# Optimization experiments

Hardware: AMD Instinct MI355X
Metric: run time of the kernel (lower is better)

The kernel has to match this reference:

```python
import jax, jax.numpy as jnp
import numpy as np

T, N, E = 10, 10000, 320000
IN_C, HID_C, OUT_C = 128, 128, 64
K = 3


def _edge_weights(src, dst, n):
    # PyG ChebConv norm with sym normalization, lambda_max=2:
    # L_hat = -D^{-1/2} A D^{-1/2} (self loops removed, diagonal 0)
    valid = (src != dst).astype(jnp.float32)  # remove_self_loops
    deg = jax.ops.segment_sum(valid, src, num_segments=n)
    dinv = jnp.where(deg > 0, jax.lax.rsqrt(jnp.maximum(deg, 1.0)), 0.0)
    return -valid * dinv[src] * dinv[dst]  # [E]


def _agg(w, src, dst, x, n):
    # (L_hat @ x): messages from src to dst
    return jax.ops.segment_sum(w[:, None] * x[src], dst, num_segments=n)


def _cheb(x, W, b, w, src, dst, n):
    # ChebConv K=3: T0=x, T1=L_hat x, T2=2 L_hat T1 - T0
    Tx0 = x
    Tx1 = _agg(w, src, dst, Tx0, n)
    Tx2 = 2.0 * _agg(w, src, dst, Tx1, n) - Tx0
    return Tx0 @ W[0] + Tx1 @ W[1] + Tx2 @ W[2] + b


def setup_inputs() -> dict:
    key = jax.random.key(0)
    ks = jax.random.split(key, 20)
    features_seq = jax.random.normal(ks[0], (T, N, IN_C), dtype=jnp.float32)
    edges_seq = jax.random.randint(ks[1], (T, 2, E), 0, N, dtype=jnp.int64)
    s = 0.05
    inp = {"features_seq": features_seq, "edges_seq": edges_seq}
    names = ["Wxz", "Whz", "Wxr", "Whr", "Wxh", "Whh"]
    ins = [IN_C, HID_C, IN_C, HID_C, IN_C, HID_C]
    for i, (nm, ci) in enumerate(zip(names, ins)):
        inp[nm] = jax.random.normal(ks[2 + i], (K, ci, HID_C), dtype=jnp.float32) * s
        inp["b" + nm[1:].lower()] = jnp.zeros((HID_C,), dtype=jnp.float32)
    inp["Wp"] = jax.random.normal(ks[10], (HID_C, OUT_C), dtype=jnp.float32) * s
    inp["bp"] = jnp.zeros((OUT_C,), dtype=jnp.float32)
    return inp


def reference(features_seq, edges_seq, Wxz, bxz, Whz, bhz, Wxr, bxr, Whr, bhr,
              Wxh, bxh, Whh, bhh, Wp, bp):
    n = features_seq.shape[1]

    def step(h, xt_et):
        x, e = xt_et
        src, dst = e[0], e[1]
        w = _edge_weights(src, dst, n)
        z = jax.nn.sigmoid(_cheb(x, Wxz, bxz, w, src, dst, n)
                           + _cheb(h, Whz, bhz, w, src, dst, n))
        r = jax.nn.sigmoid(_cheb(x, Wxr, bxr, w, src, dst, n)
                           + _cheb(h, Whr, bhr, w, src, dst, n))
        h_tilde = jnp.tanh(_cheb(x, Wxh, bxh, w, src, dst, n)
                           + _cheb(h * r, Whh, bhh, w, src, dst, n))
        h_new = z * h + (1.0 - z) * h_tilde
        return h_new, None

    h0 = jnp.zeros((n, HID_C), dtype=features_seq.dtype)
    h, _ = jax.lax.scan(step, h0, (features_seq, edges_seq))
    return h @ Wp + bp
```

## Files before the change

kernel.cpp:

```cpp
#include <hip/hip_runtime.h>

#define T_STEPS 10
#define NN 10000
#define EE 320000
#define CC 128
#define NC (NN*CC)
#define BHIST 32
#define EPB (EE/BHIST)
#define NCHK 40
#define PRS 8
#define PES 4
#define PROWS (NN/PRS)
#define PEDG (EE/PES)

typedef unsigned short u16;
typedef unsigned int u32;
typedef __attribute__((ext_vector_type(8))) short bf16x8;
typedef __attribute__((ext_vector_type(4))) float f32x4;

__device__ __forceinline__ float sigmoidf_(float x){ return 1.f/(1.f+__expf(-x)); }
__device__ __forceinline__ float tanhf_(float x){
  x = fminf(15.f, fmaxf(-15.f, x));
  float e = __expf(2.f*x);
  return (e-1.f)/(e+1.f);
}
__device__ __forceinline__ u16 f2bf(float f){
  u32 u = __float_as_uint(f);
  u32 r = u + 0x7fffu + ((u>>16)&1u);
  return (u16)(r>>16);
}
__device__ __forceinline__ float bf2f(u16 s){
  return __uint_as_float(((u32)s)<<16);
}
__device__ __forceinline__ float blo(u32 u){ return __uint_as_float(u<<16); }
__device__ __forceinline__ float bhi(u32 u){ return __uint_as_float(u & 0xffff0000u); }
__device__ __forceinline__ void gload16(const void* g, void* l){
  __builtin_amdgcn_global_load_lds(
    (const __attribute__((address_space(1))) void*)g,
    (__attribute__((address_space(3))) void*)l, 16, 0, 0);
}

__global__ __launch_bounds__(256) void prep_kernel(
    const float* __restrict__ Wxz, const float* __restrict__ Whz,
    const float* __restrict__ Wxr, const float* __restrict__ Whr,
    const float* __restrict__ Wxh, const float* __restrict__ Whh,
    const float* __restrict__ bxz, const float* __restrict__ bhz,
    const float* __restrict__ bxr, const float* __restrict__ bhr,
    const float* __restrict__ bxh, const float* __restrict__ bhh,
    const float* __restrict__ Wp,
    u16* __restrict__ WbigT, u16* __restrict__ WrT, u16* __restrict__ WpT,
    float* __restrict__ bz, float* __restrict__ br, float* __restrict__ bht,
    u16* __restrict__ h)
{
  int idx = blockIdx.x*256 + threadIdx.x;
  if (idx < NC) h[idx] = 0;
  if (idx < 384*768) {
    int c = idx / 768, k = idx - c*768;
    int gate = c >> 7, cc = c & 127;
    int hside = (k >= 384);
    int kk = hside ? k - 384 : k;
    int blk = kk >> 7, row = kk & 127;
    const float* W = nullptr;
    if (!hside) W = (gate==0) ? Wxz : (gate==1) ? Wxr : Wxh;
    else if (gate==0) W = Whz; else if (gate==1) W = Whr;
    float v = 0.f;
    if (W) {
      int base = row*CC + cc;
      float w0 = W[base], w1 = W[CC*CC + base], w2 = W[2*CC*CC + base];
      v = (blk==0) ? (w0 - w2) : (blk==1) ? w1 : (2.f*w2);
    }
    WbigT[idx] = f2bf(v);
  }
  if (idx < 128*384) {
    int c = idx / 384, k = idx - c*384;
    int blk = k >> 7, row = k & 127;
    int base = row*CC + c;
    float w0 = Whh[base], w1 = Whh[CC*CC+base], w2 = Whh[2*CC*CC+base];
    WrT[idx] = f2bf((blk==0) ? (w0-w2) : (blk==1) ? w1 : (2.f*w2));
  }
  if (idx < 64*128) {
    int c = idx >> 7, k = idx & 127;
    WpT[idx] = f2bf(Wp[k*64 + c]);
  }
  if (idx < CC) {
    bz[idx]  = bxz[idx] + bhz[idx];
    br[idx]  = bxr[idx] + bhr[idx];
    bht[idx] = bxh[idx] + bhh[idx];
  }
}

__global__ __launch_bounds__(256) void xconv_kernel(const float* __restrict__ x, u16* __restrict__ xb, int n4){
  int i = blockIdx.x*256 + threadIdx.x;
  if (i >= n4) return;
  long long o = (long long)i*4;
  float4 v = *(const float4*)(x + o);
  u32 u0 = (u32)f2bf(v.x) | ((u32)f2bf(v.y)<<16);
  u32 u1 = (u32)f2bf(v.z) | ((u32)f2bf(v.w)<<16);
  uint2 r; r.x=u0; r.y=u1;
  *(uint2*)(xb + o) = r;
}

__global__ __launch_bounds__(512) void hist_kernel(const int* __restrict__ edges,
                                                   u32* __restrict__ histP){
  __shared__ u32 hist[NN];
  int t = blockIdx.y, b = blockIdx.x, tid = threadIdx.x;
  for (int i = tid; i < NN; i += 512) hist[i] = 0;
  __syncthreads();
  const int* src = edges + (size_t)t*2*EE;
  const int* dst = src + EE;
  int e1 = b*EPB + EPB;
  #pragma unroll 4
  for (int e = b*EPB + tid; e < e1; e += 512){
    int s = src[e], d = dst[e];
    if (s != d){
      atomicAdd(&hist[s], 1u);
      atomicAdd(&hist[d], 1u << 16);
    }
  }
  __syncthreads();
  u32* hp = histP + ((size_t)t*BHIST + b)*NN;
  for (int i = tid; i < NN; i += 512) hp[i] = hist[i];
}

__global__ __launch_bounds__(256) void reduce_scan_kernel(u32* __restrict__ histP,
                                                          int* __restrict__ rowptr_all,
                                                          int* __restrict__ chunk_tot,
                                                          float* __restrict__ dinv_all){
  int t = blockIdx.y, ch = blockIdx.x, tid = threadIdx.x;
  int d = ch*256 + tid;
  u32 run=0, degs=0;
  if (d < NN){
    size_t base = (size_t)t*BHIST*NN + d;
    #pragma unroll
    for (int b=0;b<BHIST;++b){
      size_t ix = base + (size_t)b*NN;
      u32 v = histP[ix];
      histP[ix] = (v & 0xffffu) | (run<<16);
      run += v>>16;
      degs += v & 0xffffu;
    }
    dinv_all[t*NN+d] = degs>0 ? rsqrtf((float)degs) : 0.f;
  }
  int lane = tid&63, wv = tid>>6;
  int s = (int)run;
  #pragma unroll
  for (int off=1; off<64; off<<=1){
    int u = __shfl_up(s, off, 64);
    if (lane>=off) s += u;
  }
  __shared__ int wsum[4];
  if (lane==63) wsum[wv] = s;
  __syncthreads();
  int add = 0;
  #pragma unroll
  for (int w=0; w<3; ++w) if (w < wv) add += wsum[w];
  int incl = s + add;
  if (d < NN) rowptr_all[(size_t)t*(NN+1)+d] = incl - (int)run;
  if (tid==255) chunk_tot[t*NCHK + ch] = incl;
}

__global__ __launch_bounds__(64) void scanb_kernel(const int* __restrict__ chunk_tot,
                                                   int* __restrict__ chunk_base,
                                                   int* __restrict__ rowptr_all){
  int t = blockIdx.x; int lane = threadIdx.x;
  int v = (lane < NCHK) ? chunk_tot[t*NCHK+lane] : 0;
  int s = v;
  #pragma unroll
  for (int off=1; off<64; off<<=1){
    int u = __shfl_up(s, off, 64);
    if (lane>=off) s += u;
  }
  if (lane < NCHK) chunk_base[t*NCHK+lane] = s - v;
  if (lane == NCHK-1) rowptr_all[(size_t)t*(NN+1)+NN] = s;
}

__global__ __launch_bounds__(256) void scanc_kernel(int* __restrict__ rowptr_all,
                                                    const int* __restrict__ chunk_base){
  int t = blockIdx.y, ch = blockIdx.x;
  int d = ch*256 + threadIdx.x;
  if (d < NN) rowptr_all[(size_t)t*(NN+1)+d] += chunk_base[t*NCHK+ch];
}

__global__ __launch_bounds__(512) void place_kernel(const int* __restrict__ edges,
                                                    const int* __restrict__ rowptr_all,
                                                    const u32* __restrict__ histP,
                                                    u16* __restrict__ colA_all){
  __shared__ int slot[PROWS];
  int t = blockIdx.y, b = blockIdx.x, tid = threadIdx.x;
  int rs = b >> 2, es = b & 3;
  int lo = rs*PROWS, hi = lo + PROWS;
  const int* rowptr = rowptr_all + (size_t)t*(NN+1);
  const u32* hp = histP + ((size_t)t*BHIST + es*8)*NN;
  for (int i = tid; i < PROWS; i += 512)
    slot[i] = rowptr[lo+i] + (int)(hp[lo+i] >> 16);
  __syncthreads();
  const int* src = edges + (size_t)t*2*EE;
  const int* dst = src + EE;
  u16* colA = colA_all + (size_t)t*EE;
  int e1 = es*PEDG + PEDG;
  #pragma unroll 4
  for (int e = es*PEDG + tid; e < e1; e += 512){
    int d = dst[e];
    if (d >= lo && d < hi){
      int s = src[e];
      if (s != d){
        int pos = atomicAdd(&slot[d-lo], 1);
        colA[pos] = (u16)s;
      }
    }
  }
}

__device__ __forceinline__ void spmm_row4(const int* __restrict__ rowptr, const u16* __restrict__ colA,
                                          const float* __restrict__ dinv,
                                          const u16* __restrict__ in, u16* __restrict__ out,
                                          int wb, int wave, int lane){
  int row = wb*4 + wave;
  int k0 = rowptr[row], k1 = rowptr[row+1];
  int q = lane >> 4, cl = lane & 15;
  float a0=0.f,a1=0.f,a2=0.f,a3=0.f,a4=0.f,a5=0.f,a6=0.f,a7=0.f;
  #pragma unroll 2
  for (int k = k0 + q; k < k1; k += 4){
    int s = colA[k];
    float w = dinv[s];
    uint4 u = *(const uint4*)(in + (size_t)s*CC + cl*8);
    a0 = fmaf(w, blo(u.x), a0);  a1 = fmaf(w, bhi(u.x), a1);
    a2 = fmaf(w, blo(u.y), a2);  a3 = fmaf(w, bhi(u.y), a3);
    a4 = fmaf(w, blo(u.z), a4);  a5 = fmaf(w, bhi(u.z), a5);
    a6 = fmaf(w, blo(u.w), a6);  a7 = fmaf(w, bhi(u.w), a7);
  }
  a0 += __shfl_xor(a0,16); a1 += __shfl_xor(a1,16);
  a2 += __shfl_xor(a2,16); a3 += __shfl_xor(a3,16);
  a4 += __shfl_xor(a4,16); a5 += __shfl_xor(a5,16);
  a6 += __shfl_xor(a6,16); a7 += __shfl_xor(a7,16);
  a0 += __shfl_xor(a0,32); a1 += __shfl_xor(a1,32);
  a2 += __shfl_xor(a2,32); a3 += __shfl_xor(a3,32);
  a4 += __shfl_xor(a4,32); a5 += __shfl_xor(a5,32);
  a6 += __shfl_xor(a6,32); a7 += __shfl_xor(a7,32);
  if (q == 0){
    float wrow = -dinv[row];
    uint4 r;
    r.x = (u32)f2bf(wrow*a0) | ((u32)f2bf(wrow*a1)<<16);
    r.y = (u32)f2bf(wrow*a2) | ((u32)f2bf(wrow*a3)<<16);
    r.z = (u32)f2bf(wrow*a4) | ((u32)f2bf(wrow*a5)<<16);
    r.w = (u32)f2bf(wrow*a6) | ((u32)f2bf(wrow*a7)<<16);
    *(uint4*)(out + (size_t)row*CC + cl*8) = r;
  }
}

__global__ __launch_bounds__(256) void spmm_kernel(const int* __restrict__ rowptr, const u16* __restrict__ colA,
                                                   const float* __restrict__ dinv,
                                                   const u16* __restrict__ in, u16* __restrict__ out){
  int wave = threadIdx.x >> 6, lane = threadIdx.x & 63;
  int wb = blockIdx.x;
  if (wb >= NN/4) return;
  spmm_row4(rowptr, colA, dinv, in, out, wb, wave, lane);
}

__global__ __launch_bounds__(256) void spmm2_kernel(const int* __restrict__ rowptr, const u16* __restrict__ colA,
                                                    const float* __restrict__ dinv,
                                                    const u16* __restrict__ in0, u16* __restrict__ out0,
                                                    const u16* __restrict__ in1, u16* __restrict__ out1){
  int wave = threadIdx.x >> 6, lane = threadIdx.x & 63;
  int bid = blockIdx.x;
  int xcd = bid & 7;
  int inp = xcd >> 2;
  int wb  = (bid >> 3)*4 + (xcd & 3);
  if (wb >= NN/4) return;
  spmm_row4(rowptr, colA, dinv, inp?in1:in0, inp?out1:out0, wb, wave, lane);
}

template<int NSEG, int KDIM, int EPI, int SWZN>
__global__ __launch_bounds__(256) void mgemm_kernel(
    const u16* __restrict__ A0, const u16* __restrict__ A1, const u16* __restrict__ A2,
    const u16* __restrict__ A3, const u16* __restrict__ A4, const u16* __restrict__ A5,
    const u16* __restrict__ Bt,
    const float* __restrict__ bias0, const float* __restrict__ bias1,
    const u16* __restrict__ hbuf,
    float* __restrict__ zbuf, float* __restrict__ chx,
    u16* __restrict__ hr_out, u16* __restrict__ h_out,
    float* __restrict__ out_f)
{
  __shared__ __align__(16) u16 As[64*128];
  __shared__ __align__(16) u16 Bs[64*128];
  const u16* segs[6] = {A0,A1,A2,A3,A4,A5};
  int tid = threadIdx.x, lane = tid & 63, wvi = tid >> 6;
  int m0, n0;
  if (SWZN > 0){
    int bid = blockIdx.x;
    int j = bid >> 3;
    int mt = (bid & 7)*20 + (j % 20);
    if (mt >= 157) return;
    m0 = mt*64; n0 = (j/20)*64;
  } else {
    m0 = blockIdx.x*64; n0 = blockIdx.y*64;
  }
  int wr = wvi >> 1, wc = wvi & 1;

  f32x4 acc[2][2] = {};

  int c_lo = wvi*64 + lane;
  int rl = lane & 15, rg = lane >> 4;
  int offA[2][4], offB[2][4];
  #pragma unroll
  for (int mf=0; mf<2; ++mf)
    #pragma unroll
    for (int ks=0; ks<4; ++ks){
      offA[mf][ks] = (wr*32 + mf*16 + rl)*256 + ((((ks<<2)+rg) ^ rl)<<4);
      offB[mf][ks] = (wc*32 + mf*16 + rl)*256 + ((((ks<<2)+rg) ^ rl)<<4);
    }

  const int ktend = (EPI==1 && n0 >= 256) ? (NSEG/2) : NSEG;
  for (int kt=0; kt<ktend; ++kt){
    const u16* __restrict__ Aseg = segs[kt];
    __syncthreads();
    #pragma unroll
    for (int i=0;i<4;++i){
      int c = i*256 + c_lo;
      int row = c >> 4, slot = c & 15;
      int scw = slot ^ (row & 15);
      int grow = m0 + row; if (grow > NN-1) grow = NN-1;
      gload16(Aseg + (size_t)grow*CC + scw*8,
              (u16*)As + ((size_t)i*256 + wvi*64)*8);
      gload16(Bt + (size_t)(n0 + row)*KDIM + kt*128 + scw*8,
              (u16*)Bs + ((size_t)i*256 + wvi*64)*8);
    }
    __syncthreads();
    #pragma unroll
    for (int ks=0; ks<4; ++ks){
      bf16x8 a0 = *(const bf16x8*)((const char*)As + offA[0][ks]);
      bf16x8 a1 = *(const bf16x8*)((const char*)As + offA[1][ks]);
      bf16x8 b0 = *(const bf16x8*)((const char*)Bs + offB[0][ks]);
      bf16x8 b1 = *(const bf16x8*)((const char*)Bs + offB[1][ks]);
      acc[0][0] = __builtin_amdgcn_mfma_f32_16x16x32_bf16(a0, b0, acc[0][0], 0,0,0);
      acc[0][1] = __builtin_amdgcn_mfma_f32_16x16x32_bf16(a0, b1, acc[0][1], 0,0,0);
      acc[1][0] = __builtin_amdgcn_mfma_f32_16x16x32_bf16(a1, b0, acc[1][0], 0,0,0);
      acc[1][1] = __builtin_amdgcn_mfma_f32_16x16x32_bf16(a1, b1, acc[1][1], 0,0,0);
    }
  }

  #pragma unroll
  for (int mf=0; mf<2; ++mf){
    #pragma unroll
    for (int nf=0; nf<2; ++nf){
      #pragma unroll
      for (int r=0; r<4; ++r){
        int grow = m0 + wr*32 + mf*16 + rg*4 + r;
        if (grow >= NN) continue;
        int gcol = n0 + wc*32 + nf*16 + rl;
        float v = acc[mf][nf][r];
        if (EPI==0){
          out_f[(size_t)grow*64 + gcol] = v + bias0[gcol];
        } else if (EPI==1){
          int gate = gcol >> 7, c = gcol & 127;
          size_t idx = (size_t)grow*CC + c;
          if (gate==0)      zbuf[idx] = sigmoidf_(v + bias0[c]);
          else if (gate==1){
            float rr = sigmoidf_(v + bias1[c]);
            hr_out[idx] = f2bf(rr * bf2f(hbuf[idx]));
          } else            chx[idx] = v;
        } else {
          size_t idx = (size_t)grow*CC + gcol;
          float pre = v + chx[idx] + bias0[gcol];
          float ht = tanhf_(pre);
          float zz = zbuf[idx];
          float hv = bf2f(hbuf[idx]);
          h_out[idx] = f2bf(fmaf(zz, hv - ht, ht));
        }
      }
    }
  }
}

extern "C" void kernel_launch(void* const* d_in, const int* in_sizes, int n_in,
                              void* d_out, int out_size, void* d_ws, size_t ws_size,
                              hipStream_t stream)
{
  (void)in_sizes; (void)n_in; (void)out_size; (void)ws_size;
  const float* feat = (const float*)d_in[0];
  const int*   edges = (const int*)d_in[1];
  const float* Wxz=(const float*)d_in[2];  const float* bxz=(const float*)d_in[3];
  const float* Whz=(const float*)d_in[4];  const float* bhz=(const float*)d_in[5];
  const float* Wxr=(const float*)d_in[6];  const float* bxr=(const float*)d_in[7];
  const float* Whr=(const float*)d_in[8];  const float* bhr=(const float*)d_in[9];
  const float* Wxh=(const float*)d_in[10]; const float* bxh=(const float*)d_in[11];
  const float* Whh=(const float*)d_in[12]; const float* bhh=(const float*)d_in[13];
  const float* Wp =(const float*)d_in[14]; const float* bp =(const float*)d_in[15];
  float* out = (float*)d_out;

  char* p = (char*)d_ws;
  auto alloc = [&](size_t bytes)->char* {
    char* r = p; p += (bytes + 255) & ~(size_t)255; return r;
  };
  u16* xb   = (u16*)alloc((size_t)T_STEPS*NC*2);
  u16* h    = (u16*)alloc((size_t)NC*2);
  u16* a1x  = (u16*)alloc((size_t)NC*2);
  u16* a2x  = (u16*)alloc((size_t)NC*2);
  u16* a1h  = (u16*)alloc((size_t)NC*2);
  u16* a2h  = (u16*)alloc((size_t)NC*2);
  u16* hr   = (u16*)alloc((size_t)NC*2);
  float* zbuf = (float*)alloc((size_t)NC*4);
  float* chx  = (float*)alloc((size_t)NC*4);
  u16* WbigT = (u16*)alloc(384*768*2);
  u16* WrT   = (u16*)alloc(128*384*2);
  u16* WpT   = (u16*)alloc(64*128*2);
  float* bz  = (float*)alloc(CC*4);
  float* br  = (float*)alloc(CC*4);
  float* bht = (float*)alloc(CC*4);
  float* dinv_all = (float*)alloc((size_t)T_STEPS*NN*4);
  int* rowptr_all = (int*)alloc((size_t)T_STEPS*(NN+1)*4);
  u16* colA_all   = (u16*)alloc((size_t)T_STEPS*EE*2);
  int* chunk_tot  = (int*)alloc((size_t)T_STEPS*NCHK*4);
  int* chunk_base = (int*)alloc((size_t)T_STEPS*NCHK*4);
  u32* histP = (u32*)hr;

  prep_kernel<<<NC/256, 256, 0, stream>>>(Wxz,Whz,Wxr,Whr,Wxh,Whh,
                                          bxz,bhz,bxr,bhr,bxh,bhh, Wp,
                                          WbigT, WrT, WpT, bz, br, bht, h);
  xconv_kernel<<<(T_STEPS*NC/4 + 255)/256, 256, 0, stream>>>(feat, xb, T_STEPS*NC/4);

  hist_kernel<<<dim3(BHIST, T_STEPS), 512, 0, stream>>>(edges, histP);
  reduce_scan_kernel<<<dim3(NCHK, T_STEPS), 256, 0, stream>>>(histP, rowptr_all, chunk_tot, dinv_all);
  scanb_kernel<<<T_STEPS, 64, 0, stream>>>(chunk_tot, chunk_base, rowptr_all);
  scanc_kernel<<<dim3(NCHK, T_STEPS), 256, 0, stream>>>(rowptr_all, chunk_base);
  place_kernel<<<dim3(PRS*PES, T_STEPS), 512, 0, stream>>>(edges, rowptr_all, histP, colA_all);

  for (int t=0; t<T_STEPS; ++t){
    const int*   rowptr = rowptr_all + (size_t)t*(NN+1);
    const u16*   colA   = colA_all + (size_t)t*EE;
    const float* dinv   = dinv_all + (size_t)t*NN;
    const u16*   x      = xb + (size_t)t*NC;

    spmm2_kernel<<<dim3(2*(NN/4)), 256, 0, stream>>>(rowptr,colA,dinv, x,a1x, h,a1h);
    spmm2_kernel<<<dim3(2*(NN/4)), 256, 0, stream>>>(rowptr,colA,dinv, a1x,a2x, a1h,a2h);

    mgemm_kernel<6,768,1,6><<<dim3(8*20*6), 256, 0, stream>>>(
        x,a1x,a2x,h,a1h,a2h, WbigT, bz, br, h, zbuf, chx, hr, nullptr, nullptr);

    spmm_kernel<<<dim3(NN/4), 256, 0, stream>>>(rowptr,colA,dinv, hr, a1x);
    spmm_kernel<<<dim3(NN/4), 256, 0, stream>>>(rowptr,colA,dinv, a1x, a2x);

    mgemm_kernel<3,384,2,2><<<dim3(8*20*2), 256, 0, stream>>>(
        hr,a1x,a2x,nullptr,nullptr,nullptr, WrT, bht, nullptr, h, zbuf, chx,
        nullptr, h, nullptr);
  }

  mgemm_kernel<1,128,0,0><<<dim3(157,1), 256, 0, stream>>>(
      h,nullptr,nullptr,nullptr,nullptr,nullptr, WpT, bp, nullptr,
      nullptr, nullptr, nullptr, nullptr, nullptr, out);
}
```

Before: 923.7 us.

## Batch input-feature Chebyshev aggregations for all timesteps before the recurrent loop

The x-side sparse aggregations (L_hat x and L_hat^2 x) do not depend on the hidden state, so they are hoisted out of the time loop and computed for all ten timesteps in two large batched launches, with per-timestep result buffers. Inside the loop only the hidden-state aggregations remain, run with the single-input spmm kernel. Separately, the edge placement kernel now gives each block a full-row shared slot table and its own edge chunk, replacing the row-range/edge-split scheme. This trades extra workspace memory for fewer serial small launches and better GPU fill, and changes the parallel decomposition of placement.

Result: faster. 898.8 us (-2.7%).

```diff
diff --git a/kernel.cpp b/kernel.cpp
--- a/kernel.cpp
+++ b/kernel.cpp
@@ -8,10 +8,6 @@
 #define BHIST 32
 #define EPB (EE/BHIST)
 #define NCHK 40
-#define PRS 8
-#define PES 4
-#define PROWS (NN/PRS)
-#define PEDG (EE/PES)
 
 typedef unsigned short u16;
 typedef unsigned int u32;
@@ -185,28 +181,22 @@
                                                     const int* __restrict__ rowptr_all,
                                                     const u32* __restrict__ histP,
                                                     u16* __restrict__ colA_all){
-  __shared__ int slot[PROWS];
+  __shared__ int slot[NN];
   int t = blockIdx.y, b = blockIdx.x, tid = threadIdx.x;
-  int rs = b >> 2, es = b & 3;
-  int lo = rs*PROWS, hi = lo + PROWS;
   const int* rowptr = rowptr_all + (size_t)t*(NN+1);
-  const u32* hp = histP + ((size_t)t*BHIST + es*8)*NN;
-  for (int i = tid; i < PROWS; i += 512)
-    slot[i] = rowptr[lo+i] + (int)(hp[lo+i] >> 16);
+  const u32* hp = histP + ((size_t)t*BHIST + b)*NN;
+  for (int i = tid; i < NN; i += 512) slot[i] = rowptr[i] + (int)(hp[i] >> 16);
   __syncthreads();
   const int* src = edges + (size_t)t*2*EE;
   const int* dst = src + EE;
   u16* colA = colA_all + (size_t)t*EE;
-  int e1 = es*PEDG + PEDG;
+  int e1 = b*EPB + EPB;
   #pragma unroll 4
-  for (int e = es*PEDG + tid; e < e1; e += 512){
-    int d = dst[e];
-    if (d >= lo && d < hi){
-      int s = src[e];
-      if (s != d){
-        int pos = atomicAdd(&slot[d-lo], 1);
-        colA[pos] = (u16)s;
-      }
+  for (int e = b*EPB + tid; e < e1; e += 512){
+    int s = src[e], d = dst[e];
+    if (s != d){
+      int pos = atomicAdd(&slot[d], 1);
+      colA[pos] = (u16)s;
     }
   }
 }
@@ -257,17 +247,23 @@
   spmm_row4(rowptr, colA, dinv, in, out, wb, wave, lane);
 }
 
-__global__ __launch_bounds__(256) void spmm2_kernel(const int* __restrict__ rowptr, const u16* __restrict__ colA,
-                                                    const float* __restrict__ dinv,
-                                                    const u16* __restrict__ in0, u16* __restrict__ out0,
-                                                    const u16* __restrict__ in1, u16* __restrict__ out1){
-  int wave = threadIdx.x >> 6, lane = threadIdx.x & 63;
+__global__ __launch_bounds__(256) void bxchain_kernel(const int* __restrict__ rowptr_all,
+                                                      const u16* __restrict__ colA_all,
+                                                      const float* __restrict__ dinv_all,
+                                                      const u16* __restrict__ in_all,
+                                                      u16* __restrict__ out_all){
+  int lane = threadIdx.x & 63, wave = threadIdx.x >> 6;
   int bid = blockIdx.x;
   int xcd = bid & 7;
-  int inp = xcd >> 2;
-  int wb  = (bid >> 3)*4 + (xcd & 3);
-  if (wb >= NN/4) return;
-  spmm_row4(rowptr, colA, dinv, inp?in1:in0, inp?out1:out0, wb, wave, lane);
+  int j = bid >> 3;
+  int t, wb;
+  if (j < 2500){ t = xcd; wb = j; }
+  else { t = 8 + (xcd >> 2); wb = (j - 2500)*4 + (xcd & 3); }
+  const int*   rowptr = rowptr_all + (size_t)t*(NN+1);
+  const u16*   colA   = colA_all + (size_t)t*EE;
+  const float* dinv   = dinv_all + (size_t)t*NN;
+  spmm_row4(rowptr, colA, dinv, in_all + (size_t)t*NC, out_all + (size_t)t*NC,
+            wb, wave, lane);
 }
 
 template<int NSEG, int KDIM, int EPI, int SWZN>
@@ -392,10 +388,10 @@
   auto alloc = [&](size_t bytes)->char* {
     char* r = p; p += (bytes + 255) & ~(size_t)255; return r;
   };
-  u16* xb   = (u16*)alloc((size_t)T_STEPS*NC*2);
+  u16* xb     = (u16*)alloc((size_t)T_STEPS*NC*2);
+  u16* a1xA   = (u16*)alloc((size_t)T_STEPS*NC*2);
+  u16* a2xA   = (u16*)alloc((size_t)T_STEPS*NC*2);
   u16* h    = (u16*)alloc((size_t)NC*2);
-  u16* a1x  = (u16*)alloc((size_t)NC*2);
-  u16* a2x  = (u16*)alloc((size_t)NC*2);
   u16* a1h  = (u16*)alloc((size_t)NC*2);
   u16* a2h  = (u16*)alloc((size_t)NC*2);
   u16* hr   = (u16*)alloc((size_t)NC*2);
@@ -423,16 +419,21 @@
   reduce_scan_kernel<<<dim3(NCHK, T_STEPS), 256, 0, stream>>>(histP, rowptr_all, chunk_tot, dinv_all);
   scanb_kernel<<<T_STEPS, 64, 0, stream>>>(chunk_tot, chunk_base, rowptr_all);
   scanc_kernel<<<dim3(NCHK, T_STEPS), 256, 0, stream>>>(rowptr_all, chunk_base);
-  place_kernel<<<dim3(PRS*PES, T_STEPS), 512, 0, stream>>>(edges, rowptr_all, histP, colA_all);
+  place_kernel<<<dim3(BHIST, T_STEPS), 512, 0, stream>>>(edges, rowptr_all, histP, colA_all);
+
+  bxchain_kernel<<<dim3(25000), 256, 0, stream>>>(rowptr_all, colA_all, dinv_all, xb, a1xA);
+  bxchain_kernel<<<dim3(25000), 256, 0, stream>>>(rowptr_all, colA_all, dinv_all, a1xA, a2xA);
 
   for (int t=0; t<T_STEPS; ++t){
     const int*   rowptr = rowptr_all + (size_t)t*(NN+1);
     const u16*   colA   = colA_all + (size_t)t*EE;
     const float* dinv   = dinv_all + (size_t)t*NN;
     const u16*   x      = xb + (size_t)t*NC;
-
-    spmm2_kernel<<<dim3(2*(NN/4)), 256, 0, stream>>>(rowptr,colA,dinv, x,a1x, h,a1h);
-    spmm2_kernel<<<dim3(2*(NN/4)), 256, 0, stream>>>(rowptr,colA,dinv, a1x,a2x, a1h,a2h);
+    u16* a1x = a1xA + (size_t)t*NC;
+    u16* a2x = a2xA + (size_t)t*NC;
+
+    spmm_kernel<<<dim3(NN/4), 256, 0, stream>>>(rowptr,colA,dinv, h, a1h);
+    spmm_kernel<<<dim3(NN/4), 256, 0, stream>>>(rowptr,colA,dinv, a1h, a2h);
 
     mgemm_kernel<6,768,1,6><<<dim3(8*20*6), 256, 0, stream>>>(
         x,a1x,a2x,h,a1h,a2h, WbigT, bz, br, h, zbuf, chx, hr, nullptr, nullptr);
```

## Simplify edge placement to per-histogram-block slots and widen SpMM lane work to 16 channels

Applied to the files above, without the earlier changes.

The place kernel stops partitioning by row range and edge slice. Each block now handles one histogram block's edge chunk, keeps slot counters for all 10000 rows in shared memory (40KB), and drops the per-edge row-range filter. The SpMM row routine now has each lane cover 16 channels with two 16-byte loads and walk 8 edges in parallel instead of 4, adding one more shuffle-reduction level. The intent is fewer redundant edge reads during placement and more memory parallelism per wave in the gather. The costs are higher register pressure from 16 accumulators and lower occupancy for the place kernel because of its large shared array.

Result: faster. 883.6 us (-4.3%).

```diff
diff --git a/kernel.cpp b/kernel.cpp
--- a/kernel.cpp
+++ b/kernel.cpp
@@ -8,10 +8,6 @@
 #define BHIST 32
 #define EPB (EE/BHIST)
 #define NCHK 40
-#define PRS 8
-#define PES 4
-#define PROWS (NN/PRS)
-#define PEDG (EE/PES)
 
 typedef unsigned short u16;
 typedef unsigned int u32;
@@ -185,28 +181,22 @@
                                                     const int* __restrict__ rowptr_all,
                                                     const u32* __restrict__ histP,
                                                     u16* __restrict__ colA_all){
-  __shared__ int slot[PROWS];
+  __shared__ int slot[NN];
   int t = blockIdx.y, b = blockIdx.x, tid = threadIdx.x;
-  int rs = b >> 2, es = b & 3;
-  int lo = rs*PROWS, hi = lo + PROWS;
   const int* rowptr = rowptr_all + (size_t)t*(NN+1);
-  const u32* hp = histP + ((size_t)t*BHIST + es*8)*NN;
-  for (int i = tid; i < PROWS; i += 512)
-    slot[i] = rowptr[lo+i] + (int)(hp[lo+i] >> 16);
+  const u32* hp = histP + ((size_t)t*BHIST + b)*NN;
+  for (int i = tid; i < NN; i += 512) slot[i] = rowptr[i] + (int)(hp[i] >> 16);
   __syncthreads();
   const int* src = edges + (size_t)t*2*EE;
   const int* dst = src + EE;
   u16* colA = colA_all + (size_t)t*EE;
-  int e1 = es*PEDG + PEDG;
+  int e1 = b*EPB + EPB;
   #pragma unroll 4
-  for (int e = es*PEDG + tid; e < e1; e += 512){
-    int d = dst[e];
-    if (d >= lo && d < hi){
-      int s = src[e];
-      if (s != d){
-        int pos = atomicAdd(&slot[d-lo], 1);
-        colA[pos] = (u16)s;
-      }
+  for (int e = b*EPB + tid; e < e1; e += 512){
+    int s = src[e], d = dst[e];
+    if (s != d){
+      int pos = atomicAdd(&slot[d], 1);
+      colA[pos] = (u16)s;
     }
   }
 }
@@ -217,34 +207,45 @@
                                           int wb, int wave, int lane){
   int row = wb*4 + wave;
   int k0 = rowptr[row], k1 = rowptr[row+1];
-  int q = lane >> 4, cl = lane & 15;
-  float a0=0.f,a1=0.f,a2=0.f,a3=0.f,a4=0.f,a5=0.f,a6=0.f,a7=0.f;
+  int q = lane >> 3, cl = lane & 7;
+  float a[16];
+  #pragma unroll
+  for (int i=0;i<16;++i) a[i]=0.f;
   #pragma unroll 2
-  for (int k = k0 + q; k < k1; k += 4){
+  for (int k = k0 + q; k < k1; k += 8){
     int s = colA[k];
     float w = dinv[s];
-    uint4 u = *(const uint4*)(in + (size_t)s*CC + cl*8);
-    a0 = fmaf(w, blo(u.x), a0);  a1 = fmaf(w, bhi(u.x), a1);
-    a2 = fmaf(w, blo(u.y), a2);  a3 = fmaf(w, bhi(u.y), a3);
-    a4 = fmaf(w, blo(u.z), a4);  a5 = fmaf(w, bhi(u.z), a5);
-    a6 = fmaf(w, blo(u.w), a6);  a7 = fmaf(w, bhi(u.w), a7);
-  }
-  a0 += __shfl_xor(a0,16); a1 += __shfl_xor(a1,16);
-  a2 += __shfl_xor(a2,16); a3 += __shfl_xor(a3,16);
-  a4 += __shfl_xor(a4,16); a5 += __shfl_xor(a5,16);
-  a6 += __shfl_xor(a6,16); a7 += __shfl_xor(a7,16);
-  a0 += __shfl_xor(a0,32); a1 += __shfl_xor(a1,32);
-  a2 += __shfl_xor(a2,32); a3 += __shfl_xor(a3,32);
-  a4 += __shfl_xor(a4,32); a5 += __shfl_xor(a5,32);
-  a6 += __shfl_xor(a6,32); a7 += __shfl_xor(a7,32);
+    const u16* pr = in + (size_t)s*CC + cl*16;
+    uint4 u = *(const uint4*)pr;
+    uint4 v = *(const uint4*)(pr + 8);
+    a[0] = fmaf(w, blo(u.x), a[0]);  a[1] = fmaf(w, bhi(u.x), a[1]);
+    a[2] = fmaf(w, blo(u.y), a[2]);  a[3] = fmaf(w, bhi(u.y), a[3]);
+    a[4] = fmaf(w, blo(u.z), a[4]);  a[5] = fmaf(w, bhi(u.z), a[5]);
+    a[6] = fmaf(w, blo(u.w), a[6]);  a[7] = fmaf(w, bhi(u.w), a[7]);
+    a[8] = fmaf(w, blo(v.x), a[8]);  a[9] = fmaf(w, bhi(v.x), a[9]);
+    a[10]= fmaf(w, blo(v.y), a[10]); a[11]= fmaf(w, bhi(v.y), a[11]);
+    a[12]= fmaf(w, blo(v.z), a[12]); a[13]= fmaf(w, bhi(v.z), a[13]);
+    a[14]= fmaf(w, blo(v.w), a[14]); a[15]= fmaf(w, bhi(v.w), a[15]);
+  }
+  #pragma unroll
+  for (int m = 8; m <= 32; m <<= 1){
+    #pragma unroll
+    for (int i=0;i<16;++i) a[i] += __shfl_xor(a[i], m);
+  }
   if (q == 0){
     float wrow = -dinv[row];
-    uint4 r;
-    r.x = (u32)f2bf(wrow*a0) | ((u32)f2bf(wrow*a1)<<16);
-    r.y = (u32)f2bf(wrow*a2) | ((u32)f2bf(wrow*a3)<<16);
-    r.z = (u32)f2bf(wrow*a4) | ((u32)f2bf(wrow*a5)<<16);
-    r.w = (u32)f2bf(wrow*a6) | ((u32)f2bf(wrow*a7)<<16);
-    *(uint4*)(out + (size_t)row*CC + cl*8) = r;
+    uint4 r0, r1;
+    r0.x = (u32)f2bf(wrow*a[0])  | ((u32)f2bf(wrow*a[1])<<16);
+    r0.y = (u32)f2bf(wrow*a[2])  | ((u32)f2bf(wrow*a[3])<<16);
+    r0.z = (u32)f2bf(wrow*a[4])  | ((u32)f2bf(wrow*a[5])<<16);
+    r0.w = (u32)f2bf(wrow*a[6])  | ((u32)f2bf(wrow*a[7])<<16);
+    r1.x = (u32)f2bf(wrow*a[8])  | ((u32)f2bf(wrow*a[9])<<16);
+    r1.y = (u32)f2bf(wrow*a[10]) | ((u32)f2bf(wrow*a[11])<<16);
+    r1.z = (u32)f2bf(wrow*a[12]) | ((u32)f2bf(wrow*a[13])<<16);
+    r1.w = (u32)f2bf(wrow*a[14]) | ((u32)f2bf(wrow*a[15])<<16);
+    u16* po = out + (size_t)row*CC + cl*16;
+    *(uint4*)po = r0;
+    *(uint4*)(po + 8) = r1;
   }
 }
 
@@ -423,7 +424,7 @@
   reduce_scan_kernel<<<dim3(NCHK, T_STEPS), 256, 0, stream>>>(histP, rowptr_all, chunk_tot, dinv_all);
   scanb_kernel<<<T_STEPS, 64, 0, stream>>>(chunk_tot, chunk_base, rowptr_all);
   scanc_kernel<<<dim3(NCHK, T_STEPS), 256, 0, stream>>>(rowptr_all, chunk_base);
-  place_kernel<<<dim3(PRS*PES, T_STEPS), 512, 0, stream>>>(edges, rowptr_all, histP, colA_all);
+  place_kernel<<<dim3(BHIST, T_STEPS), 512, 0, stream>>>(edges, rowptr_all, histP, colA_all);
 
   for (int t=0; t<T_STEPS; ++t){
     const int*   rowptr = rowptr_all + (size_t)t*(NN+1);
```
